# Performance work log

Hardware: AMD Instinct MI355X
Metric: run time of the kernel (lower is better)

The kernel has to match this reference:

```python
import jax, jax.numpy as jnp
import numpy as np

K = 1024
D = 64
N = 262144

def setup_inputs() -> dict:
    key = jax.random.key(0)
    k1, k2 = jax.random.split(key)
    z_e = jax.random.normal(k1, (N, D), dtype=jnp.float32)
    # nn.Embedding weight init: uniform(-1/K, 1/K)
    codebook = jax.random.uniform(k2, (K, D), dtype=jnp.float32, minval=-1.0 / K, maxval=1.0 / K)
    return {"z_e": z_e, "codebook": codebook}

def reference(z_e, codebook):
    # torch.cdist -> Euclidean distances; argmin over squared distances is identical
    # and avoids the sqrt. dist2[n,k] = ||z_e[n]||^2 - 2 z_e@cb^T + ||cb[k]||^2
    ze_sq = jnp.sum(z_e * z_e, axis=1, keepdims=True)            # [N,1]
    cb_sq = jnp.sum(codebook * codebook, axis=1)                  # [K]
    dist2 = ze_sq - 2.0 * (z_e @ codebook.T) + cb_sq[None, :]     # [N,K]
    encoding_inds = jnp.argmin(dist2, axis=1)                     # [N]
    z_q = codebook[encoding_inds]                                 # [N,D] gather
    return (z_q, encoding_inds)
```

## Files before the change

kernel.cpp:

```cpp
#include <hip/hip_runtime.h>


#define VQ_D 64
#define VQ_MAXK 1024

typedef __attribute__((ext_vector_type(4))) float f4;
typedef const __attribute__((address_space(4))) f4* cb4c_t;
typedef const __attribute__((address_space(4))) float* fc_t;

#define VQ_CH2(qa, qb, c) do { \
    s0 = fmaf((qa).x, (c).x, s0); s1 = fmaf((qb).x, (c).x, s1); \
    s0 = fmaf((qa).y, (c).y, s0); s1 = fmaf((qb).y, (c).y, s1); \
    s0 = fmaf((qa).z, (c).z, s0); s1 = fmaf((qb).z, (c).z, s1); \
    s0 = fmaf((qa).w, (c).w, s0); s1 = fmaf((qb).w, (c).w, s1); } while (0)

#define VQ_SQ(acc, q) do { \
    (acc) += (double)(q).x * (double)(q).x; \
    (acc) += (double)(q).y * (double)(q).y; \
    (acc) += (double)(q).z * (double)(q).z; \
    (acc) += (double)(q).w * (double)(q).w; } while (0)

#define SBAR() __builtin_amdgcn_sched_barrier(0)

__global__ void vq_cbsq_kernel(const float* __restrict__ cb,
                               float* __restrict__ cbsq, int K)
{
    const int k = blockIdx.x * blockDim.x + threadIdx.x;
    if (k >= K) return;
    const float* c = cb + (size_t)k * VQ_D;
    double s = 0.0;
    #pragma unroll
    for (int d = 0; d < VQ_D; ++d) { double v = (double)c[d]; s += v * v; }
    cbsq[k] = (float)s;
}

template <bool USE_WS>
__global__ __launch_bounds__(256, 2) void vq_argmin_kernel(
    const float* __restrict__ z_e,
    const float* __restrict__ cb,
    const float* __restrict__ cbsq_ws,
    float* __restrict__ out,
    int N, int K)
{
    __shared__ float s_cbsq[VQ_MAXK];

    if (!USE_WS) {
        for (int k = threadIdx.x; k < K; k += blockDim.x) {
            const float* c = cb + (size_t)k * VQ_D;
            double s = 0.0;
            #pragma unroll
            for (int d = 0; d < VQ_D; ++d) { double v = (double)c[d]; s += v * v; }
            s_cbsq[k] = (float)s;
        }
        __syncthreads();
    }

    int n0 = blockIdx.x * (2 * (int)blockDim.x) + threadIdx.x;
    if (n0 >= N) return;
    int n1 = n0 + (int)blockDim.x;
    if (n1 >= N) n1 = n0;

    const float4* zp0 = (const float4*)(z_e + (size_t)n0 * VQ_D);
    const float4* zp1 = (const float4*)(z_e + (size_t)n1 * VQ_D);
    float4 a0  = zp0[0],  a1  = zp0[1],  a2  = zp0[2],  a3  = zp0[3];
    float4 a4  = zp0[4],  a5  = zp0[5],  a6  = zp0[6],  a7  = zp0[7];
    float4 a8  = zp0[8],  a9  = zp0[9],  a10 = zp0[10], a11 = zp0[11];
    float4 a12 = zp0[12], a13 = zp0[13], a14 = zp0[14], a15 = zp0[15];
    float4 b0  = zp1[0],  b1  = zp1[1],  b2  = zp1[2],  b3  = zp1[3];
    float4 b4  = zp1[4],  b5  = zp1[5],  b6  = zp1[6],  b7  = zp1[7];
    float4 b8  = zp1[8],  b9  = zp1[9],  b10 = zp1[10], b11 = zp1[11];
    float4 b12 = zp1[12], b13 = zp1[13], b14 = zp1[14], b15 = zp1[15];

    double zs0 = 0.0, zs1 = 0.0;
    VQ_SQ(zs0, a0);  VQ_SQ(zs0, a1);  VQ_SQ(zs0, a2);  VQ_SQ(zs0, a3);
    VQ_SQ(zs0, a4);  VQ_SQ(zs0, a5);  VQ_SQ(zs0, a6);  VQ_SQ(zs0, a7);
    VQ_SQ(zs0, a8);  VQ_SQ(zs0, a9);  VQ_SQ(zs0, a10); VQ_SQ(zs0, a11);
    VQ_SQ(zs0, a12); VQ_SQ(zs0, a13); VQ_SQ(zs0, a14); VQ_SQ(zs0, a15);
    VQ_SQ(zs1, b0);  VQ_SQ(zs1, b1);  VQ_SQ(zs1, b2);  VQ_SQ(zs1, b3);
    VQ_SQ(zs1, b4);  VQ_SQ(zs1, b5);  VQ_SQ(zs1, b6);  VQ_SQ(zs1, b7);
    VQ_SQ(zs1, b8);  VQ_SQ(zs1, b9);  VQ_SQ(zs1, b10); VQ_SQ(zs1, b11);
    VQ_SQ(zs1, b12); VQ_SQ(zs1, b13); VQ_SQ(zs1, b14); VQ_SQ(zs1, b15);
    const float zsq0 = (float)zs0;
    const float zsq1 = (float)zs1;

    cb4c_t cbc = (cb4c_t)(unsigned long long)cb;
    fc_t   sqc = (fc_t)(unsigned long long)cbsq_ws;

    float best0 = 3.4e38f, best1 = 3.4e38f;
    int bk0 = 0, bk1 = 0;

    f4 X0, X1, X2, X3, X4, X5, X6, X7;
    f4 Y0, Y1, Y2, Y3, Y4, Y5, Y6, Y7;
    float cq;

    X0 = cbc[0]; X1 = cbc[1]; X2 = cbc[2]; X3 = cbc[3];
    X4 = cbc[4]; X5 = cbc[5]; X6 = cbc[6]; X7 = cbc[7];

    #pragma unroll 1
    for (int k = 0; k < K; ++k) {
        const int kb = k << 4;
        float s0 = 0.f, s1 = 0.f;

        VQ_CH2(a0, b0, X0);
        SBAR();
        Y0 = cbc[kb + 8];  Y1 = cbc[kb + 9];  Y2 = cbc[kb + 10]; Y3 = cbc[kb + 11];
        Y4 = cbc[kb + 12]; Y5 = cbc[kb + 13]; Y6 = cbc[kb + 14]; Y7 = cbc[kb + 15];
        cq = USE_WS ? sqc[k] : s_cbsq[k];
        SBAR();
        VQ_CH2(a1, b1, X1); VQ_CH2(a2, b2, X2); VQ_CH2(a3, b3, X3);
        VQ_CH2(a4, b4, X4); VQ_CH2(a5, b5, X5); VQ_CH2(a6, b6, X6);
        VQ_CH2(a7, b7, X7);

        VQ_CH2(a8, b8, Y0);
        SBAR();
        {
            int nk = k + 1; if (nk >= K) nk = K - 1;
            const int nb = nk << 4;
            X0 = cbc[nb + 0]; X1 = cbc[nb + 1]; X2 = cbc[nb + 2]; X3 = cbc[nb + 3];
            X4 = cbc[nb + 4]; X5 = cbc[nb + 5]; X6 = cbc[nb + 6]; X7 = cbc[nb + 7];
        }
        SBAR();
        VQ_CH2(a9,  b9,  Y1); VQ_CH2(a10, b10, Y2); VQ_CH2(a11, b11, Y3);
        VQ_CH2(a12, b12, Y4); VQ_CH2(a13, b13, Y5); VQ_CH2(a14, b14, Y6);
        VQ_CH2(a15, b15, Y7);

        const float u0    = zsq0 - 2.0f * s0;
        const float dist0 = u0 + cq;
        const float u1    = zsq1 - 2.0f * s1;
        const float dist1 = u1 + cq;
        if (dist0 < best0) { best0 = dist0; bk0 = k; }
        if (dist1 < best1) { best1 = dist1; bk1 = k; }
    }

    {
        const float4* cq0 = (const float4*)(cb + (size_t)bk0 * VQ_D);
        float4* oq0 = (float4*)(out + (size_t)n0 * VQ_D);
        #pragma unroll
        for (int i = 0; i < VQ_D / 4; ++i) oq0[i] = cq0[i];
        const float4* cq1 = (const float4*)(cb + (size_t)bk1 * VQ_D);
        float4* oq1 = (float4*)(out + (size_t)n1 * VQ_D);
        #pragma unroll
        for (int i = 0; i < VQ_D / 4; ++i) oq1[i] = cq1[i];
    }

    out[(size_t)N * VQ_D + n0] = (float)bk0;
    out[(size_t)N * VQ_D + n1] = (float)bk1;
}

extern "C" void kernel_launch(void* const* d_in, const int* in_sizes, int n_in,
                              void* d_out, int out_size, void* d_ws, size_t ws_size,
                              hipStream_t stream) {
    const float* z_e = (const float*)d_in[0];
    const float* cb  = (const float*)d_in[1];
    float* out = (float*)d_out;

    const int N = in_sizes[0] / VQ_D;
    const int K = in_sizes[1] / VQ_D;

    const int block = 256;
    const int rows_per_block = 2 * block;
    const int grid = (N + rows_per_block - 1) / rows_per_block;

    const bool use_ws = (d_ws != nullptr) && (ws_size >= (size_t)K * sizeof(float));
    if (use_ws) {
        float* cbsq = (float*)d_ws;
        vq_cbsq_kernel<<<(K + 255) / 256, 256, 0, stream>>>(cb, cbsq, K);
        vq_argmin_kernel<true><<<grid, block, 0, stream>>>(z_e, cb, cbsq, out, N, K);
    } else {
        vq_argmin_kernel<false><<<grid, block, 0, stream>>>(z_e, cb, nullptr, out, N, K);
    }
}
```

Measured before the change: 584.1 us.

## Process one row per thread and raise occupancy to four blocks per CU

Each thread now computes the nearest codeword for a single row instead of two, halving the register footprint for query data. The launch bound is raised to allow four blocks per CU, and the grid doubles. The aim is to hide load latency with more waves, at the cost of amortizing each scalar codebook load over half as many FMAs.

New measurement: 735.4 us. +25.9%, slower.

```diff
diff --git a/kernel.cpp b/kernel.cpp
--- a/kernel.cpp
+++ b/kernel.cpp
@@ -8,11 +8,11 @@
 typedef const __attribute__((address_space(4))) f4* cb4c_t;
 typedef const __attribute__((address_space(4))) float* fc_t;
 
-#define VQ_CH2(qa, qb, c) do { \
-    s0 = fmaf((qa).x, (c).x, s0); s1 = fmaf((qb).x, (c).x, s1); \
-    s0 = fmaf((qa).y, (c).y, s0); s1 = fmaf((qb).y, (c).y, s1); \
-    s0 = fmaf((qa).z, (c).z, s0); s1 = fmaf((qb).z, (c).z, s1); \
-    s0 = fmaf((qa).w, (c).w, s0); s1 = fmaf((qb).w, (c).w, s1); } while (0)
+#define VQ_CH1(q, c) do { \
+    s0 = fmaf((q).x, (c).x, s0); \
+    s0 = fmaf((q).y, (c).y, s0); \
+    s0 = fmaf((q).z, (c).z, s0); \
+    s0 = fmaf((q).w, (c).w, s0); } while (0)
 
 #define VQ_SQ(acc, q) do { \
     (acc) += (double)(q).x * (double)(q).x; \
@@ -35,7 +35,7 @@
 }
 
 template <bool USE_WS>
-__global__ __launch_bounds__(256, 2) void vq_argmin_kernel(
+__global__ __launch_bounds__(256, 4) void vq_argmin_kernel(
     const float* __restrict__ z_e,
     const float* __restrict__ cb,
     const float* __restrict__ cbsq_ws,
@@ -55,39 +55,27 @@
         __syncthreads();
     }
 
-    int n0 = blockIdx.x * (2 * (int)blockDim.x) + threadIdx.x;
-    if (n0 >= N) return;
-    int n1 = n0 + (int)blockDim.x;
-    if (n1 >= N) n1 = n0;
+    const int n = blockIdx.x * blockDim.x + threadIdx.x;
+    if (n >= N) return;
 
-    const float4* zp0 = (const float4*)(z_e + (size_t)n0 * VQ_D);
-    const float4* zp1 = (const float4*)(z_e + (size_t)n1 * VQ_D);
-    float4 a0  = zp0[0],  a1  = zp0[1],  a2  = zp0[2],  a3  = zp0[3];
-    float4 a4  = zp0[4],  a5  = zp0[5],  a6  = zp0[6],  a7  = zp0[7];
-    float4 a8  = zp0[8],  a9  = zp0[9],  a10 = zp0[10], a11 = zp0[11];
-    float4 a12 = zp0[12], a13 = zp0[13], a14 = zp0[14], a15 = zp0[15];
-    float4 b0  = zp1[0],  b1  = zp1[1],  b2  = zp1[2],  b3  = zp1[3];
-    float4 b4  = zp1[4],  b5  = zp1[5],  b6  = zp1[6],  b7  = zp1[7];
-    float4 b8  = zp1[8],  b9  = zp1[9],  b10 = zp1[10], b11 = zp1[11];
-    float4 b12 = zp1[12], b13 = zp1[13], b14 = zp1[14], b15 = zp1[15];
+    const float4* zp = (const float4*)(z_e + (size_t)n * VQ_D);
+    float4 q0  = zp[0],  q1  = zp[1],  q2  = zp[2],  q3  = zp[3];
+    float4 q4  = zp[4],  q5  = zp[5],  q6  = zp[6],  q7  = zp[7];
+    float4 q8  = zp[8],  q9  = zp[9],  q10 = zp[10], q11 = zp[11];
+    float4 q12 = zp[12], q13 = zp[13], q14 = zp[14], q15 = zp[15];
 
-    double zs0 = 0.0, zs1 = 0.0;
-    VQ_SQ(zs0, a0);  VQ_SQ(zs0, a1);  VQ_SQ(zs0, a2);  VQ_SQ(zs0, a3);
-    VQ_SQ(zs0, a4);  VQ_SQ(zs0, a5);  VQ_SQ(zs0, a6);  VQ_SQ(zs0, a7);
-    VQ_SQ(zs0, a8);  VQ_SQ(zs0, a9);  VQ_SQ(zs0, a10); VQ_SQ(zs0, a11);
-    VQ_SQ(zs0, a12); VQ_SQ(zs0, a13); VQ_SQ(zs0, a14); VQ_SQ(zs0, a15);
-    VQ_SQ(zs1, b0);  VQ_SQ(zs1, b1);  VQ_SQ(zs1, b2);  VQ_SQ(zs1, b3);
-    VQ_SQ(zs1, b4);  VQ_SQ(zs1, b5);  VQ_SQ(zs1, b6);  VQ_SQ(zs1, b7);
-    VQ_SQ(zs1, b8);  VQ_SQ(zs1, b9);  VQ_SQ(zs1, b10); VQ_SQ(zs1, b11);
-    VQ_SQ(zs1, b12); VQ_SQ(zs1, b13); VQ_SQ(zs1, b14); VQ_SQ(zs1, b15);
-    const float zsq0 = (float)zs0;
-    const float zsq1 = (float)zs1;
+    double zs0 = 0.0;
+    VQ_SQ(zs0, q0);  VQ_SQ(zs0, q1);  VQ_SQ(zs0, q2);  VQ_SQ(zs0, q3);
+    VQ_SQ(zs0, q4);  VQ_SQ(zs0, q5);  VQ_SQ(zs0, q6);  VQ_SQ(zs0, q7);
+    VQ_SQ(zs0, q8);  VQ_SQ(zs0, q9);  VQ_SQ(zs0, q10); VQ_SQ(zs0, q11);
+    VQ_SQ(zs0, q12); VQ_SQ(zs0, q13); VQ_SQ(zs0, q14); VQ_SQ(zs0, q15);
+    const float zsq = (float)zs0;
 
     cb4c_t cbc = (cb4c_t)(unsigned long long)cb;
     fc_t   sqc = (fc_t)(unsigned long long)cbsq_ws;
 
-    float best0 = 3.4e38f, best1 = 3.4e38f;
-    int bk0 = 0, bk1 = 0;
+    float best = 3.4e38f;
+    int bestk = 0;
 
     f4 X0, X1, X2, X3, X4, X5, X6, X7;
     f4 Y0, Y1, Y2, Y3, Y4, Y5, Y6, Y7;
@@ -99,19 +87,18 @@
     #pragma unroll 1
     for (int k = 0; k < K; ++k) {
         const int kb = k << 4;
-        float s0 = 0.f, s1 = 0.f;
+        float s0 = 0.f;
 
-        VQ_CH2(a0, b0, X0);
+        VQ_CH1(q0, X0);
         SBAR();
         Y0 = cbc[kb + 8];  Y1 = cbc[kb + 9];  Y2 = cbc[kb + 10]; Y3 = cbc[kb + 11];
         Y4 = cbc[kb + 12]; Y5 = cbc[kb + 13]; Y6 = cbc[kb + 14]; Y7 = cbc[kb + 15];
         cq = USE_WS ? sqc[k] : s_cbsq[k];
         SBAR();
-        VQ_CH2(a1, b1, X1); VQ_CH2(a2, b2, X2); VQ_CH2(a3, b3, X3);
-        VQ_CH2(a4, b4, X4); VQ_CH2(a5, b5, X5); VQ_CH2(a6, b6, X6);
-        VQ_CH2(a7, b7, X7);
+        VQ_CH1(q1, X1); VQ_CH1(q2, X2); VQ_CH1(q3, X3);
+        VQ_CH1(q4, X4); VQ_CH1(q5, X5); VQ_CH1(q6, X6); VQ_CH1(q7, X7);
 
-        VQ_CH2(a8, b8, Y0);
+        VQ_CH1(q8, Y0);
         SBAR();
         {
             int nk = k + 1; if (nk >= K) nk = K - 1;
@@ -120,31 +107,20 @@
             X4 = cbc[nb + 4]; X5 = cbc[nb + 5]; X6 = cbc[nb + 6]; X7 = cbc[nb + 7];
         }
         SBAR();
-        VQ_CH2(a9,  b9,  Y1); VQ_CH2(a10, b10, Y2); VQ_CH2(a11, b11, Y3);
-        VQ_CH2(a12, b12, Y4); VQ_CH2(a13, b13, Y5); VQ_CH2(a14, b14, Y6);
-        VQ_CH2(a15, b15, Y7);
+        VQ_CH1(q9,  Y1); VQ_CH1(q10, Y2); VQ_CH1(q11, Y3);
+        VQ_CH1(q12, Y4); VQ_CH1(q13, Y5); VQ_CH1(q14, Y6); VQ_CH1(q15, Y7);
 
-        const float u0    = zsq0 - 2.0f * s0;
-        const float dist0 = u0 + cq;
-        const float u1    = zsq1 - 2.0f * s1;
-        const float dist1 = u1 + cq;
-        if (dist0 < best0) { best0 = dist0; bk0 = k; }
-        if (dist1 < best1) { best1 = dist1; bk1 = k; }
+        const float u    = zsq - 2.0f * s0;
+        const float dist = u + cq;
+        if (dist < best) { best = dist; bestk = k; }
     }
 
-    {
-        const float4* cq0 = (const float4*)(cb + (size_t)bk0 * VQ_D);
-        float4* oq0 = (float4*)(out + (size_t)n0 * VQ_D);
-        #pragma unroll
-        for (int i = 0; i < VQ_D / 4; ++i) oq0[i] = cq0[i];
-        const float4* cq1 = (const float4*)(cb + (size_t)bk1 * VQ_D);
-        float4* oq1 = (float4*)(out + (size_t)n1 * VQ_D);
-        #pragma unroll
-        for (int i = 0; i < VQ_D / 4; ++i) oq1[i] = cq1[i];
-    }
+    const float4* cq4 = (const float4*)(cb + (size_t)bestk * VQ_D);
+    float4* oq = (float4*)(out + (size_t)n * VQ_D);
+    #pragma unroll
+    for (int i = 0; i < VQ_D / 4; ++i) oq[i] = cq4[i];
 
-    out[(size_t)N * VQ_D + n0] = (float)bk0;
-    out[(size_t)N * VQ_D + n1] = (float)bk1;
+    out[(size_t)N * VQ_D + n] = (float)bestk;
 }
 
 extern "C" void kernel_launch(void* const* d_in, const int* in_sizes, int n_in,
@@ -158,8 +134,7 @@
     const int K = in_sizes[1] / VQ_D;
 
     const int block = 256;
-    const int rows_per_block = 2 * block;
-    const int grid = (N + rows_per_block - 1) / rows_per_block;
+    const int grid = (N + block - 1) / block;
 
     const bool use_ws = (d_ws != nullptr) && (ws_size >= (size_t)K * sizeof(float));
     if (use_ws) {
```

## Split codebook loads across scalar and vector paths with two-row software pipeline

Applied to the files above, without the earlier changes.

Unrolls the codebook loop by two and double-buffers the codebook rows. The first half of each row is still read through scalar (constant address space) loads, while the second half now comes through ordinary vector global loads prefetched up to two iterations ahead. The aim is to ease the scalar-load bottleneck and hide load latency behind the FMA chain. In exchange it uses many more VGPRs for the prefetched float4 registers, which may lower occupancy, and it assumes K is even.

After: 1.677 ms. +187.1%, slower.

```diff
diff --git a/kernel.cpp b/kernel.cpp
--- a/kernel.cpp
+++ b/kernel.cpp
@@ -85,51 +85,94 @@
 
     cb4c_t cbc = (cb4c_t)(unsigned long long)cb;
     fc_t   sqc = (fc_t)(unsigned long long)cbsq_ws;
+    const float4* cbv = (const float4*)cb;
 
     float best0 = 3.4e38f, best1 = 3.4e38f;
     int bk0 = 0, bk1 = 0;
 
-    f4 X0, X1, X2, X3, X4, X5, X6, X7;
-    f4 Y0, Y1, Y2, Y3, Y4, Y5, Y6, Y7;
-    float cq;
-
-    X0 = cbc[0]; X1 = cbc[1]; X2 = cbc[2]; X3 = cbc[3];
-    X4 = cbc[4]; X5 = cbc[5]; X6 = cbc[6]; X7 = cbc[7];
+    f4 P0, P1, P2, P3, P4, P5, P6, P7;
+    f4 Q0, Q1, Q2, Q3, Q4, Q5, Q6, Q7;
+    float cqP, cqQ;
+    float4 Vc0, Vc1, Vc2, Vc3, Vc4, Vc5, Vc6, Vc7;
+    float4 Vn0, Vn1, Vn2, Vn3, Vn4, Vn5, Vn6, Vn7;
+
+    P0 = cbc[0]; P1 = cbc[1]; P2 = cbc[2]; P3 = cbc[3];
+    P4 = cbc[4]; P5 = cbc[5]; P6 = cbc[6]; P7 = cbc[7];
+    cqP = USE_WS ? sqc[0] : s_cbsq[0];
+    {
+        const float4* g0 = cbv + 8;
+        Vc0 = g0[0]; Vc1 = g0[1]; Vc2 = g0[2]; Vc3 = g0[3];
+        Vc4 = g0[4]; Vc5 = g0[5]; Vc6 = g0[6]; Vc7 = g0[7];
+        const float4* g1 = cbv + 16 + 8;
+        Vn0 = g1[0]; Vn1 = g1[1]; Vn2 = g1[2]; Vn3 = g1[3];
+        Vn4 = g1[4]; Vn5 = g1[5]; Vn6 = g1[6]; Vn7 = g1[7];
+    }
 
     #pragma unroll 1
-    for (int k = 0; k < K; ++k) {
-        const int kb = k << 4;
-        float s0 = 0.f, s1 = 0.f;
-
-        VQ_CH2(a0, b0, X0);
-        SBAR();
-        Y0 = cbc[kb + 8];  Y1 = cbc[kb + 9];  Y2 = cbc[kb + 10]; Y3 = cbc[kb + 11];
-        Y4 = cbc[kb + 12]; Y5 = cbc[kb + 13]; Y6 = cbc[kb + 14]; Y7 = cbc[kb + 15];
-        cq = USE_WS ? sqc[k] : s_cbsq[k];
-        SBAR();
-        VQ_CH2(a1, b1, X1); VQ_CH2(a2, b2, X2); VQ_CH2(a3, b3, X3);
-        VQ_CH2(a4, b4, X4); VQ_CH2(a5, b5, X5); VQ_CH2(a6, b6, X6);
-        VQ_CH2(a7, b7, X7);
-
-        VQ_CH2(a8, b8, Y0);
-        SBAR();
+    for (int k = 0; k < K; k += 2) {
         {
-            int nk = k + 1; if (nk >= K) nk = K - 1;
-            const int nb = nk << 4;
-            X0 = cbc[nb + 0]; X1 = cbc[nb + 1]; X2 = cbc[nb + 2]; X3 = cbc[nb + 3];
-            X4 = cbc[nb + 4]; X5 = cbc[nb + 5]; X6 = cbc[nb + 6]; X7 = cbc[nb + 7];
+            float s0 = 0.f, s1 = 0.f;
+            VQ_CH2(a0, b0, P0);
+            SBAR();
+            {
+                const int nb = (k + 1) << 4;
+                Q0 = cbc[nb + 0]; Q1 = cbc[nb + 1]; Q2 = cbc[nb + 2]; Q3 = cbc[nb + 3];
+                Q4 = cbc[nb + 4]; Q5 = cbc[nb + 5]; Q6 = cbc[nb + 6]; Q7 = cbc[nb + 7];
+                cqQ = USE_WS ? sqc[k + 1] : s_cbsq[k + 1];
+            }
+            SBAR();
+            VQ_CH2(a1, b1, P1); VQ_CH2(a2, b2, P2); VQ_CH2(a3, b3, P3);
+            VQ_CH2(a4, b4, P4); VQ_CH2(a5, b5, P5); VQ_CH2(a6, b6, P6);
+            VQ_CH2(a7, b7, P7);
+            VQ_CH2(a8,  b8,  Vc0); VQ_CH2(a9,  b9,  Vc1);
+            VQ_CH2(a10, b10, Vc2); VQ_CH2(a11, b11, Vc3);
+            VQ_CH2(a12, b12, Vc4); VQ_CH2(a13, b13, Vc5);
+            VQ_CH2(a14, b14, Vc6); VQ_CH2(a15, b15, Vc7);
+            {
+                int nk = k + 2; if (nk >= K) nk = K - 2;
+                const float4* gp = cbv + ((size_t)nk << 4) + 8;
+                Vc0 = gp[0]; Vc1 = gp[1]; Vc2 = gp[2]; Vc3 = gp[3];
+                Vc4 = gp[4]; Vc5 = gp[5]; Vc6 = gp[6]; Vc7 = gp[7];
+            }
+            const float u0    = zsq0 - 2.0f * s0;
+            const float dist0 = u0 + cqP;
+            const float u1    = zsq1 - 2.0f * s1;
+            const float dist1 = u1 + cqP;
+            if (dist0 < best0) { best0 = dist0; bk0 = k; }
+            if (dist1 < best1) { best1 = dist1; bk1 = k; }
         }
-        SBAR();
-        VQ_CH2(a9,  b9,  Y1); VQ_CH2(a10, b10, Y2); VQ_CH2(a11, b11, Y3);
-        VQ_CH2(a12, b12, Y4); VQ_CH2(a13, b13, Y5); VQ_CH2(a14, b14, Y6);
-        VQ_CH2(a15, b15, Y7);
-
-        const float u0    = zsq0 - 2.0f * s0;
-        const float dist0 = u0 + cq;
-        const float u1    = zsq1 - 2.0f * s1;
-        const float dist1 = u1 + cq;
-        if (dist0 < best0) { best0 = dist0; bk0 = k; }
-        if (dist1 < best1) { best1 = dist1; bk1 = k; }
+        {
+            float s0 = 0.f, s1 = 0.f;
+            VQ_CH2(a0, b0, Q0);
+            SBAR();
+            {
+                int nk = k + 2; if (nk >= K) nk = K - 2;
+                const int nb = nk << 4;
+                P0 = cbc[nb + 0]; P1 = cbc[nb + 1]; P2 = cbc[nb + 2]; P3 = cbc[nb + 3];
+                P4 = cbc[nb + 4]; P5 = cbc[nb + 5]; P6 = cbc[nb + 6]; P7 = cbc[nb + 7];
+                cqP = USE_WS ? sqc[nk] : s_cbsq[nk];
+            }
+            SBAR();
+            VQ_CH2(a1, b1, Q1); VQ_CH2(a2, b2, Q2); VQ_CH2(a3, b3, Q3);
+            VQ_CH2(a4, b4, Q4); VQ_CH2(a5, b5, Q5); VQ_CH2(a6, b6, Q6);
+            VQ_CH2(a7, b7, Q7);
+            VQ_CH2(a8,  b8,  Vn0); VQ_CH2(a9,  b9,  Vn1);
+            VQ_CH2(a10, b10, Vn2); VQ_CH2(a11, b11, Vn3);
+            VQ_CH2(a12, b12, Vn4); VQ_CH2(a13, b13, Vn5);
+            VQ_CH2(a14, b14, Vn6); VQ_CH2(a15, b15, Vn7);
+            {
+                int nk = k + 3; if (nk >= K) nk = K - 1;
+                const float4* gp = cbv + ((size_t)nk << 4) + 8;
+                Vn0 = gp[0]; Vn1 = gp[1]; Vn2 = gp[2]; Vn3 = gp[3];
+                Vn4 = gp[4]; Vn5 = gp[5]; Vn6 = gp[6]; Vn7 = gp[7];
+            }
+            const float u0    = zsq0 - 2.0f * s0;
+            const float dist0 = u0 + cqQ;
+            const float u1    = zsq1 - 2.0f * s1;
+            const float dist1 = u1 + cqQ;
+            if (dist0 < best0) { best0 = dist0; bk0 = k + 1; }
+            if (dist1 < best1) { best1 = dist1; bk1 = k + 1; }
+        }
     }
 
     {
```
